# Kernel tuning notes

Hardware: AMD Instinct MI355X
Metric: run time of the kernel (lower is better)

Reference implementation:

```python
import jax, jax.numpy as jnp
import numpy as np

B, N, DIM, QK, H, GS = 4, 4096, 512, 512, 8, 128
NUM_LABELS = 8
R_BASE, R_MIN, R_MAX = 0.5, 0.25, 0.75
LAMBDA_P, LAMBDA_V, CCR = 0.25, 0.25, 0.125


def setup_inputs() -> dict:
    key = jax.random.key(0)
    ks = jax.random.split(key, 7)
    s = DIM ** -0.5
    return {
        "x": jax.random.normal(ks[0], (B, N, DIM), jnp.float32),
        "labels": jax.random.randint(ks[1], (B, N), 0, NUM_LABELS),
        "scores": jax.random.uniform(ks[2], (B, N), jnp.float32),
        "Wq": jax.random.normal(ks[3], (DIM, QK), jnp.float32) * s,
        "Wk": jax.random.normal(ks[4], (DIM, QK), jnp.float32) * s,
        "Wv": jax.random.normal(ks[5], (DIM, DIM), jnp.float32) * s,
        "Wproj": jax.random.normal(ks[6], (DIM, DIM), jnp.float32) * s,
    }


def _windows(t, gs, ng):
    # pad with flipped last-group tail, then overlapping windows of size 2*gs, stride gs
    tp = jnp.concatenate([t, jnp.flip(t[:, -gs:], axis=1)], axis=1)
    a = tp.reshape(t.shape[0], ng + 1, gs, *t.shape[2:])
    return jnp.concatenate([a[:, :-1], a[:, 1:]], axis=2)  # [b, ng, 2*gs, ...]


def _topk_mask(vals, keep, cand):
    # rank of each entry when sorted descending; keep top-`keep` among candidates
    ranks = jnp.argsort(jnp.argsort(-vals, axis=-1), axis=-1)
    return (ranks < keep[:, :, None, None, None]) & cand


def reference(x, labels, scores, Wq, Wk, Wv, Wproj):
    b, n, _ = x.shape
    gs = GS
    ng = n // gs            # num_tokens divisible by group_size -> pad_n = 0
    ws = 2 * gs
    q = x @ Wq
    k = x @ Wk
    v = x @ Wv

    qw = q.reshape(b, ng, gs, H, -1).transpose(0, 1, 3, 2, 4)          # b ng h gs d
    kw = _windows(k, gs, ng).reshape(b, ng, ws, H, -1).transpose(0, 1, 3, 2, 4)
    vw = _windows(v, gs, ng).reshape(b, ng, ws, H, -1).transpose(0, 1, 3, 2, 4)
    q_labels = labels.reshape(b, ng, gs)
    k_labels = _windows(labels, gs, ng)                                 # b ng ws
    q_scores = scores.reshape(b, ng, gs)
    k_scores = _windows(scores, gs, ng)

    d = qw.shape[-1]
    scale = 1.0 / jnp.sqrt(jnp.asarray(d, qw.dtype))
    logits = jnp.einsum('bghqd,bghkd->bghqk', qw, kw) * scale           # b ng h gs ws
    attn_hat = jax.nn.softmax(logits, axis=-1)  # no prev_attn_state -> attn_hat = attn_cur

    # dynamic focus ratio: purity from group mode label + score variance
    counts = jax.nn.one_hot(q_labels, NUM_LABELS, dtype=jnp.float32).sum(axis=2)  # b ng L
    mode = jnp.argmax(counts, axis=-1)
    purity = jnp.mean((q_labels == mode[..., None]).astype(jnp.float32), axis=-1)
    score_var = jnp.var(q_scores.astype(jnp.float32), axis=-1)  # unbiased=False
    focus = jnp.clip(R_BASE + LAMBDA_P * purity - LAMBDA_V * score_var, R_MIN, R_MAX)

    keep = jnp.clip(jnp.ceil(focus * ws).astype(jnp.int32), 1, ws)
    cross_keep = jnp.round(keep.astype(jnp.float32) * CCR).astype(jnp.int32)
    cross_keep = jnp.where(keep > 1, jnp.maximum(cross_keep, 1), 0)
    same_keep = jnp.maximum(keep - cross_keep, 1)

    same_mask = (q_labels[:, :, None, :, None] == k_labels[:, :, None, None, :])  # b ng 1 gs ws

    same_scores = jnp.where(same_mask, attn_hat, -10000.0)
    m_same = _topk_mask(same_scores, same_keep, same_mask)
    pair_conf = q_scores[:, :, None, :, None] * k_scores[:, :, None, None, :]
    cross_scores = attn_hat * pair_conf
    m_cross = _topk_mask(cross_scores, cross_keep, ~same_mask)
    final_mask = m_same | m_cross

    sparse_logits = jnp.where(final_mask, logits, -10000.0)
    attn_local = jax.nn.softmax(sparse_logits, axis=-1)
    attn_local = jnp.where(final_mask, attn_local, 0.0)
    attn_local = attn_local / (attn_local.sum(axis=-1, keepdims=True) + 1e-9)

    out = jnp.einsum('bghqk,bghkd->bghqd', attn_local, vw)
    out = out.transpose(0, 1, 3, 2, 4).reshape(b, ng * gs, -1)[:, :n]
    return out @ Wproj, attn_local
```

## Files before the change

### kernel.cpp

```cpp
#include <hip/hip_runtime.h>

#define BB 4
#define NN 4096
#define DIMM 512
#define HH 8
#define DH 64
#define GSZ 128
#define NGRP 32
#define WSZ 256
#define CHUNK 32

#define MK 8388608u
#define WK 262144u

typedef short short8 __attribute__((ext_vector_type(8)));
typedef float f32x4 __attribute__((ext_vector_type(4)));

__device__ inline unsigned short bf16rne(float f) {
  unsigned u = __float_as_uint(f);
  unsigned r = u + 0x7FFFu + ((u >> 16) & 1u);
  return (unsigned short)(r >> 16);
}
__device__ inline float bf16tof(unsigned short h) {
  return __uint_as_float(((unsigned)h) << 16);
}

__global__ __launch_bounds__(256) void split_planes(
    const float* __restrict__ X, unsigned short* __restrict__ P)
{
  unsigned idx = (blockIdx.x * 256u + threadIdx.x) * 4u;
  float4 xv = *(const float4*)&X[idx];
  float xs[4] = {xv.x, xv.y, xv.z, xv.w};
  ushort4 hv, mv, lv;
  unsigned short* hp = (unsigned short*)&hv;
  unsigned short* mp = (unsigned short*)&mv;
  unsigned short* lp = (unsigned short*)&lv;
#pragma unroll
  for (int i = 0; i < 4; ++i) {
    unsigned short h = bf16rne(xs[i]);
    float r1 = xs[i] - bf16tof(h);
    unsigned short m = bf16rne(r1);
    float r2 = r1 - bf16tof(m);
    hp[i] = h;
    mp[i] = m;
    lp[i] = bf16rne(r2);
  }
  *(ushort4*)&P[idx] = hv;
  *(ushort4*)&P[MK + idx] = mv;
  *(ushort4*)&P[2u * MK + idx] = lv;
}

__global__ __launch_bounds__(256) void split_w(
    const float* __restrict__ Wq, const float* __restrict__ Wk,
    const float* __restrict__ Wv, const float* __restrict__ Wpj,
    unsigned short* __restrict__ wqkv, unsigned short* __restrict__ wproj)
{
  unsigned e = blockIdx.x * 256u + threadIdx.x;
  int mz = e >> 18;
  unsigned rem = e & (WK - 1u);
  unsigned kk = rem >> 9, n = rem & 511u;
  const float* src = (mz == 0) ? Wq : (mz == 1) ? Wk : (mz == 2) ? Wv : Wpj;
  float w = src[kk * 512u + n];
  unsigned short h = bf16rne(w);
  float r1 = w - bf16tof(h);
  unsigned short m = bf16rne(r1);
  float r2 = r1 - bf16tof(m);
  unsigned short l = bf16rne(r2);
  unsigned o = n * 512u + kk;
  if (mz < 3) {
    unsigned short* base = wqkv + (unsigned)mz * 3u * WK;
    base[o] = h;
    base[WK + o] = m;
    base[2u * WK + o] = l;
  } else {
    wproj[o] = h;
    wproj[WK + o] = m;
  }
}

template <int NP, int NT>
__global__ __launch_bounds__(256) void mfma_gemm(
    const unsigned short* __restrict__ Ap,
    const unsigned short* __restrict__ Wp,
    float* __restrict__ C)
{
  constexpr int ta[6] = {0, 0, 1, 1, 0, 2};
  constexpr int tw[6] = {0, 1, 0, 1, 2, 0};
  const int z = blockIdx.z;
  const int n0 = blockIdx.x * 128;
  const int m0 = blockIdx.y * 128;
  const int tid = threadIdx.x;
  const int lane = tid & 63, wv = tid >> 6;
  const int wm = (wv >> 1) * 64, wn = (wv & 1) * 64;
  const int lm = lane & 15, lk = (lane >> 4) * 8;

  __shared__ unsigned short As[NP * 128 * 40];
  __shared__ unsigned short Ws[NP * 128 * 40];

  f32x4 acc[4][4];
#pragma unroll
  for (int i = 0; i < 4; ++i)
#pragma unroll
    for (int j = 0; j < 4; ++j) acc[i][j] = (f32x4){0.f, 0.f, 0.f, 0.f};

  const unsigned short* Wz = Wp + (size_t)z * NP * WK;

  for (int k0 = 0; k0 < 512; k0 += 32) {
#pragma unroll
    for (int i = 0; i < NP * 2; ++i) {
      int idx = i * 256 + tid;
      int p = idx >> 9, rem = idx & 511;
      int r = rem >> 2, cc = rem & 3;
      *(short8*)&As[p * 5120 + r * 40 + cc * 8] =
          *(const short8*)&Ap[(size_t)p * MK + (size_t)(m0 + r) * 512 + k0 + cc * 8];
      *(short8*)&Ws[p * 5120 + r * 40 + cc * 8] =
          *(const short8*)&Wz[(size_t)p * WK + (size_t)(n0 + r) * 512 + k0 + cc * 8];
    }
    __syncthreads();

    short8 a[NP][4];
#pragma unroll
    for (int p = 0; p < NP; ++p)
#pragma unroll
      for (int fm = 0; fm < 4; ++fm)
        a[p][fm] = *(const short8*)&As[p * 5120 + (wm + fm * 16 + lm) * 40 + lk];

#pragma unroll
    for (int fn = 0; fn < 4; ++fn) {
      short8 bf[NP];
#pragma unroll
      for (int p = 0; p < NP; ++p)
        bf[p] = *(const short8*)&Ws[p * 5120 + (wn + fn * 16 + lm) * 40 + lk];
#pragma unroll
      for (int fm = 0; fm < 4; ++fm) {
#pragma unroll
        for (int t = 0; t < NT; ++t)
          acc[fm][fn] = __builtin_amdgcn_mfma_f32_16x16x32_bf16(
              a[ta[t]][fm], bf[tw[t]], acc[fm][fn], 0, 0, 0);
      }
    }
    __syncthreads();
  }

  const int rq = (lane >> 4) * 4;
  float* Cz = C + (size_t)z * 8388608u;
#pragma unroll
  for (int fm = 0; fm < 4; ++fm)
#pragma unroll
    for (int fn = 0; fn < 4; ++fn) {
      int row = m0 + wm + fm * 16 + rq;
      int col = n0 + wn + fn * 16 + lm;
#pragma unroll
      for (int r = 0; r < 4; ++r)
        Cz[(size_t)(row + r) * 512 + col] = acc[fm][fn][r];
    }
}

__global__ __launch_bounds__(256) void gemm512(
    const float* __restrict__ A,
    const float* __restrict__ W0, const float* __restrict__ W1, const float* __restrict__ W2,
    float* __restrict__ C0, float* __restrict__ C1, float* __restrict__ C2)
{
  const int z = blockIdx.z;
  const float* Wm = (z == 0) ? W0 : (z == 1 ? W1 : W2);
  float* Cm = (z == 0) ? C0 : (z == 1 ? C1 : C2);
  const int n0 = blockIdx.x * 128;
  const int m0 = blockIdx.y * 128;
  const int tid = threadIdx.x;
  const int tx = tid & 15, ty = tid >> 4;

  __shared__ float As[32][132];
  __shared__ float Bs[32][132];

  float acc[8][8];
#pragma unroll
  for (int i = 0; i < 8; ++i)
#pragma unroll
    for (int j = 0; j < 8; ++j) acc[i][j] = 0.f;

  for (int k0 = 0; k0 < 512; k0 += 32) {
    {
      const int c4 = tid & 7, r = tid >> 3;
#pragma unroll
      for (int p = 0; p < 128; p += 32) {
        float4 av = *(const float4*)&A[(size_t)(m0 + r + p) * 512 + k0 + c4 * 4];
        As[c4 * 4 + 0][r + p] = av.x;
        As[c4 * 4 + 1][r + p] = av.y;
        As[c4 * 4 + 2][r + p] = av.z;
        As[c4 * 4 + 3][r + p] = av.w;
      }
      const int j4 = tid & 31, rb = tid >> 5;
#pragma unroll
      for (int p = 0; p < 32; p += 8) {
        *(float4*)&Bs[rb + p][j4 * 4] =
            *(const float4*)&Wm[(size_t)(k0 + rb + p) * 512 + n0 + j4 * 4];
      }
    }
    __syncthreads();
#pragma unroll
    for (int kk = 0; kk < 32; ++kk) {
      float4 a0 = *(const float4*)&As[kk][ty * 8];
      float4 a1 = *(const float4*)&As[kk][ty * 8 + 4];
      float4 b0 = *(const float4*)&Bs[kk][tx * 8];
      float4 b1 = *(const float4*)&Bs[kk][tx * 8 + 4];
      float av[8] = {a0.x, a0.y, a0.z, a0.w, a1.x, a1.y, a1.z, a1.w};
      float bv[8] = {b0.x, b0.y, b0.z, b0.w, b1.x, b1.y, b1.z, b1.w};
#pragma unroll
      for (int i = 0; i < 8; ++i)
#pragma unroll
        for (int j = 0; j < 8; ++j) acc[i][j] += av[i] * bv[j];
    }
    __syncthreads();
  }
#pragma unroll
  for (int i = 0; i < 8; ++i) {
    size_t row = (size_t)(m0 + ty * 8 + i);
    float4 o0 = make_float4(acc[i][0], acc[i][1], acc[i][2], acc[i][3]);
    float4 o1 = make_float4(acc[i][4], acc[i][5], acc[i][6], acc[i][7]);
    *(float4*)&Cm[row * 512 + n0 + tx * 8] = o0;
    *(float4*)&Cm[row * 512 + n0 + tx * 8 + 4] = o1;
  }
}

__device__ __forceinline__ void focus_keep(
    const int* klab, const float* kscr, int* hist8, float* s_var,
    int* s_sk, int* s_ck, int tid, int lane, int wv)
{
  if (tid < GSZ) atomicAdd(&hist8[klab[tid]], 1);
  if (wv == 0) {
    double x0 = (double)kscr[lane], x1 = (double)kscr[lane + 64];
    double s = x0 + x1;
#pragma unroll
    for (int off = 32; off > 0; off >>= 1) s += __shfl_xor(s, off);
    double mean = s * (1.0 / 128.0);
    double d0 = x0 - mean, d1 = x1 - mean;
    double vs = d0 * d0 + d1 * d1;
#pragma unroll
    for (int off = 32; off > 0; off >>= 1) vs += __shfl_xor(vs, off);
    if (lane == 0) *s_var = (float)(vs * (1.0 / 128.0));
  }
  __syncthreads();
  if (tid == 0) {
    int bc = hist8[0];
    for (int l = 1; l < 8; ++l)
      if (hist8[l] > bc) bc = hist8[l];
    float purity = (float)bc * (1.0f / GSZ);
    float focus = 0.5f + 0.25f * purity - 0.25f * (*s_var);
    focus = fminf(fmaxf(focus, 0.25f), 0.75f);
    int keep = (int)ceilf(focus * (float)WSZ);
    keep = min(max(keep, 1), WSZ);
    int ck = keep >> 3, rem = keep & 7;
    if (rem > 4 || (rem == 4 && (ck & 1))) ck++;
    if (ck < 1) ck = 1;
    int sk = keep - ck;
    if (sk < 1) sk = 1;
    *s_sk = sk;
    *s_ck = ck;
  }
  __syncthreads();
}

__device__ __forceinline__ void rank_rows(
    float att[CHUNK][WSZ + 4], const int* klab, const float* kscr,
    int r0, int same_keep, int cross_keep, int lane, int wv)
{
  int kl0[4];
  float ks0[4];
#pragma unroll
  for (int m = 0; m < 4; ++m) {
    kl0[m] = klab[lane + 64 * m];
    ks0[m] = kscr[lane + 64 * m];
  }
  for (int sp = 0; sp < 4; ++sp) {
    const int rA = wv * 8 + 2 * sp, rB = rA + 1;
    const int qLA = klab[r0 + rA], qLB = klab[r0 + rB];
    const float qSA = kscr[r0 + rA], qSB = kscr[r0 + rB];
    float aA[4], aB[4];
    float mxA = -INFINITY, mxB = -INFINITY;
#pragma unroll
    for (int m = 0; m < 4; ++m) {
      aA[m] = att[rA][lane + 64 * m];
      aB[m] = att[rB][lane + 64 * m];
      mxA = fmaxf(mxA, aA[m]);
      mxB = fmaxf(mxB, aB[m]);
    }
#pragma unroll
    for (int off = 32; off > 0; off >>= 1) {
      mxA = fmaxf(mxA, __shfl_xor(mxA, off));
      mxB = fmaxf(mxB, __shfl_xor(mxB, off));
    }
    unsigned fsA[4], fcA[4], fsB[4], fcB[4];
    bool cdA[4], cdB[4];
#pragma unroll
    for (int m = 0; m < 4; ++m) {
      aA[m] = expf(aA[m] - mxA);
      aB[m] = expf(aB[m] - mxB);
      cdA[m] = (kl0[m] == qLA);
      cdB[m] = (kl0[m] == qLB);
      fsA[m] = cdA[m] ? __float_as_uint(aA[m]) : 0u;
      fsB[m] = cdB[m] ? __float_as_uint(aB[m]) : 0u;
      fcA[m] = __float_as_uint(aA[m] * (qSA * ks0[m]));
      fcB[m] = __float_as_uint(aB[m] * (qSB * ks0[m]));
    }
    unsigned tsA = 0, tcA = 0, tsB = 0, tcB = 0;
    for (int bit = 29; bit >= 0; --bit) {
      unsigned csA = tsA | (1u << bit), ccA = tcA | (1u << bit);
      unsigned csB = tsB | (1u << bit), ccB = tcB | (1u << bit);
      int nsA = 0, ncA = 0, nsB = 0, ncB = 0;
#pragma unroll
      for (int m = 0; m < 4; ++m) {
        nsA += __popcll(__ballot(fsA[m] >= csA));
        ncA += __popcll(__ballot(fcA[m] >= ccA));
        nsB += __popcll(__ballot(fsB[m] >= csB));
        ncB += __popcll(__ballot(fcB[m] >= ccB));
      }
      if (nsA >= same_keep) tsA = csA;
      if (ncA >= cross_keep) tcA = ccA;
      if (nsB >= same_keep) tsB = csB;
      if (ncB >= cross_keep) tcB = ccB;
    }
#pragma unroll
    for (int rsel = 0; rsel < 2; ++rsel) {
      const int rr = rsel ? rB : rA;
      const unsigned ts = rsel ? tsB : tsA, tc = rsel ? tcB : tcA;
      unsigned* fs = rsel ? fsB : fsA;
      unsigned* fc = rsel ? fcB : fcA;
      float* a = rsel ? aB : aA;
      bool* cand = rsel ? cdB : cdA;
      unsigned long long beqs[4], beqc[4];
      int gts = 0, gtc = 0;
#pragma unroll
      for (int m = 0; m < 4; ++m) {
        gts += __popcll(__ballot(fs[m] > ts));
        gtc += __popcll(__ballot(fc[m] > tc));
        beqs[m] = __ballot(fs[m] == ts);
        beqc[m] = __ballot(fc[m] == tc);
      }
      const int rs = same_keep - gts, rc = cross_keep - gtc;
      float pv[4];
      float S = 0.f;
      int pres = 0, prec = 0;
#pragma unroll
      for (int m = 0; m < 4; ++m) {
        int mbs = __builtin_amdgcn_mbcnt_hi((unsigned)(beqs[m] >> 32),
                   __builtin_amdgcn_mbcnt_lo((unsigned)beqs[m], 0));
        int mbc = __builtin_amdgcn_mbcnt_hi((unsigned)(beqc[m] >> 32),
                   __builtin_amdgcn_mbcnt_lo((unsigned)beqc[m], 0));
        bool keep_s = cand[m] && ((fs[m] > ts) || ((fs[m] == ts) && (pres + mbs < rs)));
        bool keep_c = (!cand[m]) && ((fc[m] > tc) || ((fc[m] == tc) && (prec + mbc < rc)));
        pv[m] = (keep_s || keep_c) ? a[m] : 0.f;
        S += pv[m];
        pres += __popcll(beqs[m]);
        prec += __popcll(beqc[m]);
      }
#pragma unroll
      for (int off = 32; off > 0; off >>= 1) S += __shfl_xor(S, off);
      const float inv = 1.0f / S;
#pragma unroll
      for (int m = 0; m < 4; ++m) att[rr][lane + 64 * m] = pv[m] * inv;
    }
  }
}

template <int OMODE>
__global__ __launch_bounds__(256, 3) void attn_f32(
    const float* q, const float* __restrict__ k, const float* __restrict__ v,
    const int* __restrict__ labels, const float* __restrict__ scores,
    float* __restrict__ attn_out, float* o, unsigned short* __restrict__ opl)
{
  const int bx = blockIdx.x;
  const int c = bx >> 10;
  const int rblk = bx & 1023;
  const int h = rblk & 7;
  const int g = (rblk >> 3) & 31;
  const int b = rblk >> 8;
  const int r0 = c * CHUNK;
  const int tid = threadIdx.x;
  const int lane = tid & 63, wv = tid >> 6;

  __shared__ float att[CHUNK][WSZ + 4];
  __shared__ float ktile[64][DH + 4];
  __shared__ int klab[WSZ];
  __shared__ float kscr[WSZ];
  __shared__ int hist8[8];
  __shared__ float s_var;
  __shared__ int s_sk, s_ck;

  {
    int j = tid;
    int pos = g * GSZ + j;
    int tok = pos < NN ? pos : (2 * NN - 1 - pos);
    klab[j] = labels[b * NN + tok];
    kscr[j] = scores[b * NN + tok];
  }
  if (tid < 8) hist8[tid] = 0;
  __syncthreads();
  focus_keep(klab, kscr, hist8, &s_var, &s_sk, &s_ck, tid, lane, wv);
  const int same_keep = s_sk, cross_keep = s_ck;

  const int rp = tid >> 4, jx = tid & 15;
  const int srow = tid >> 4, sd4 = (tid & 15) * 4;
  const float* q0p = q + (size_t)(b * NN + g * GSZ + r0 + rp) * DIMM + h * DH;
  const float* q1p = q0p + (size_t)16 * DIMM;

  for (int jt = 0; jt < 4; ++jt) {
#pragma unroll
    for (int p = 0; p < 64; p += 16) {
      int j = jt * 64 + srow + p;
      int pos = g * GSZ + j;
      int tok = pos < NN ? pos : (2 * NN - 1 - pos);
      *(float4*)&ktile[srow + p][sd4] =
          *(const float4*)&k[(size_t)(b * NN + tok) * DIMM + h * DH + sd4];
    }
    __syncthreads();
    float acc0[4] = {0.f, 0.f, 0.f, 0.f}, acc1[4] = {0.f, 0.f, 0.f, 0.f};
#pragma unroll
    for (int dd = 0; dd < DH; dd += 4) {
      float4 q0 = *(const float4*)(q0p + dd);
      float4 q1 = *(const float4*)(q1p + dd);
#pragma unroll
      for (int jj = 0; jj < 4; ++jj) {
        float4 kv = *(const float4*)&ktile[jx + 16 * jj][dd];
        acc0[jj] += q0.x * kv.x + q0.y * kv.y + q0.z * kv.z + q0.w * kv.w;
        acc1[jj] += q1.x * kv.x + q1.y * kv.y + q1.z * kv.z + q1.w * kv.w;
      }
    }
#pragma unroll
    for (int jj = 0; jj < 4; ++jj) {
      att[rp][jt * 64 + jx + 16 * jj] = acc0[jj] * 0.125f;
      att[rp + 16][jt * 64 + jx + 16 * jj] = acc1[jj] * 0.125f;
    }
    __syncthreads();
  }

  rank_rows(att, klab, kscr, r0, same_keep, cross_keep, lane, wv);
  __syncthreads();

  {
    size_t base = ((((size_t)b * NGRP + g) * HH + h) * GSZ + r0) * WSZ;
#pragma unroll
    for (int it = 0; it < 8; ++it) {
      int idx = it * 256 + tid;
      int i = idx >> 6, j4 = (idx & 63) * 4;
      *(float4*)&attn_out[base + (size_t)i * WSZ + j4] = *(float4*)&att[i][j4];
    }
  }

  const int dx = jx;
  float oa0[4] = {0.f, 0.f, 0.f, 0.f}, oa1[4] = {0.f, 0.f, 0.f, 0.f};
  for (int jt = 0; jt < 4; ++jt) {
#pragma unroll
    for (int p = 0; p < 64; p += 16) {
      int j = jt * 64 + srow + p;
      int pos = g * GSZ + j;
      int tok = pos < NN ? pos : (2 * NN - 1 - pos);
      *(float4*)&ktile[srow + p][sd4] =
          *(const float4*)&v[(size_t)(b * NN + tok) * DIMM + h * DH + sd4];
    }
    __syncthreads();
#pragma unroll 4
    for (int jg = 0; jg < 16; ++jg) {
      float4 p0 = *(const float4*)&att[rp][jt * 64 + jg * 4];
      float4 p1 = *(const float4*)&att[rp + 16][jt * 64 + jg * 4];
      float4 v0 = *(const float4*)&ktile[jg * 4 + 0][dx * 4];
      float4 v1 = *(const float4*)&ktile[jg * 4 + 1][dx * 4];
      float4 v2 = *(const float4*)&ktile[jg * 4 + 2][dx * 4];
      float4 v3 = *(const float4*)&ktile[jg * 4 + 3][dx * 4];
      oa0[0] += p0.x * v0.x + p0.y * v1.x + p0.z * v2.x + p0.w * v3.x;
      oa0[1] += p0.x * v0.y + p0.y * v1.y + p0.z * v2.y + p0.w * v3.y;
      oa0[2] += p0.x * v0.z + p0.y * v1.z + p0.z * v2.z + p0.w * v3.z;
      oa0[3] += p0.x * v0.w + p0.y * v1.w + p0.z * v2.w + p0.w * v3.w;
      oa1[0] += p1.x * v0.x + p1.y * v1.x + p1.z * v2.x + p1.w * v3.x;
      oa1[1] += p1.x * v0.y + p1.y * v1.y + p1.z * v2.y + p1.w * v3.y;
      oa1[2] += p1.x * v0.z + p1.y * v1.z + p1.z * v2.z + p1.w * v3.z;
      oa1[3] += p1.x * v0.w + p1.y * v1.w + p1.z * v2.w + p1.w * v3.w;
    }
    __syncthreads();
  }
  if (OMODE == 0) {
    size_t ob0 = (size_t)(b * NN + g * GSZ + r0 + rp) * DIMM + h * DH + dx * 4;
    *(float4*)&o[ob0] = make_float4(oa0[0], oa0[1], oa0[2], oa0[3]);
    *(float4*)&o[ob0 + (size_t)16 * DIMM] = make_float4(oa1[0], oa1[1], oa1[2], oa1[3]);
  } else {
    size_t ob0 = (size_t)(b * NN + g * GSZ + r0 + rp) * 512 + h * 64 + dx * 4;
    ushort4 h0, m0v, h1, m1v;
    unsigned short* h0p = (unsigned short*)&h0;
    unsigned short* m0p = (unsigned short*)&m0v;
    unsigned short* h1p = (unsigned short*)&h1;
    unsigned short* m1p = (unsigned short*)&m1v;
#pragma unroll
    for (int i = 0; i < 4; ++i) {
      unsigned short hh = bf16rne(oa0[i]);
      h0p[i] = hh;
      m0p[i] = bf16rne(oa0[i] - bf16tof(hh));
      unsigned short hh1 = bf16rne(oa1[i]);
      h1p[i] = hh1;
      m1p[i] = bf16rne(oa1[i] - bf16tof(hh1));
    }
    *(ushort4*)&opl[ob0] = h0;
    *(ushort4*)&opl[MK + ob0] = m0v;
    *(ushort4*)&opl[ob0 + 16 * 512] = h1;
    *(ushort4*)&opl[MK + ob0 + 16 * 512] = m1v;
  }
}

extern "C" void kernel_launch(void* const* d_in, const int* in_sizes, int n_in,
                              void* d_out, int out_size, void* d_ws, size_t ws_size,
                              hipStream_t stream) {
  const float* x      = (const float*)d_in[0];
  const int*   labels = (const int*)d_in[1];
  const float* scores = (const float*)d_in[2];
  const float* Wq     = (const float*)d_in[3];
  const float* Wk     = (const float*)d_in[4];
  const float* Wv     = (const float*)d_in[5];
  const float* Wproj  = (const float*)d_in[6];

  float* out = (float*)d_out;
  float* attn_out = out + (size_t)BB * NN * DIMM;

  float* qb = (float*)d_ws;
  float* kb = qb + (size_t)MK;
  float* vf = kb + (size_t)MK;
  unsigned short* xpl  = (unsigned short*)(vf + (size_t)MK);
  unsigned short* wqkv = xpl + 3 * (size_t)MK;
  unsigned short* wpp  = wqkv + 9 * (size_t)WK;
  const size_t required = 3 * (size_t)MK * 4 + 3 * (size_t)MK * 2 + 11 * (size_t)WK * 2;

  if (ws_size >= required) {
    split_planes<<<dim3(MK / 1024), 256, 0, stream>>>(x, xpl);
    split_w<<<dim3(4 * WK / 256), 256, 0, stream>>>(Wq, Wk, Wv, Wproj, wqkv, wpp);
    mfma_gemm<3, 6><<<dim3(4, 128, 2), 256, 0, stream>>>(xpl, wqkv, qb);
    mfma_gemm<2, 3><<<dim3(4, 128, 1), 256, 0, stream>>>(xpl, wqkv + 6 * (size_t)WK, vf);
    attn_f32<1><<<dim3(BB * NGRP * HH * 4), 256, 0, stream>>>(
        qb, kb, vf, labels, scores, attn_out, nullptr, xpl);
    mfma_gemm<2, 3><<<dim3(4, 128, 1), 256, 0, stream>>>(xpl, wpp, out);
  } else {
    const size_t SZ = (size_t)BB * NN * DIMM;
    float* q2 = (float*)d_ws;
    float* k2 = q2 + SZ;
    float* v2 = k2 + SZ;
    gemm512<<<dim3(4, 128, 3), 256, 0, stream>>>(x, Wq, Wk, Wv, q2, k2, v2);
    attn_f32<0><<<dim3(BB * NGRP * HH * 4), 256, 0, stream>>>(
        q2, k2, v2, labels, scores, attn_out, q2, nullptr);
    gemm512<<<dim3(4, 128, 1), 256, 0, stream>>>(q2, Wproj, Wproj, Wproj, out, out, out);
  }
}
```

Baseline: 811.0 us.

## Use split-bf16 MFMA for attention-times-V and write probabilities directly

Adds a new attention kernel whose P·V product runs on bf16 MFMA with hi/lo split planes (three products) instead of scalar fp32 FMAs. V tiles are loaded, split into bf16 hi/lo and stored transposed in shared memory that aliases the K tile buffer. Probabilities are written straight from registers to global memory, and labels are stored as bytes in shared memory. This trades exact fp32 accumulation for a three-term bf16 approximation and adds conversion work and extra shared-memory traffic.

```diff
diff --git a/kernel.cpp b/kernel.cpp
--- a/kernel.cpp
+++ b/kernel.cpp
@@ -223,7 +223,7 @@
 }
 
 __device__ __forceinline__ void focus_keep(
-    const int* klab, const float* kscr, int* hist8, float* s_var,
+    const unsigned char* klab, const float* kscr, int* hist8, float* s_var,
     int* s_sk, int* s_ck, int tid, int lane, int wv)
 {
   if (tid < GSZ) atomicAdd(&hist8[klab[tid]], 1);
@@ -260,113 +260,11 @@
   __syncthreads();
 }
 
-__device__ __forceinline__ void rank_rows(
-    float att[CHUNK][WSZ + 4], const int* klab, const float* kscr,
-    int r0, int same_keep, int cross_keep, int lane, int wv)
-{
-  int kl0[4];
-  float ks0[4];
-#pragma unroll
-  for (int m = 0; m < 4; ++m) {
-    kl0[m] = klab[lane + 64 * m];
-    ks0[m] = kscr[lane + 64 * m];
-  }
-  for (int sp = 0; sp < 4; ++sp) {
-    const int rA = wv * 8 + 2 * sp, rB = rA + 1;
-    const int qLA = klab[r0 + rA], qLB = klab[r0 + rB];
-    const float qSA = kscr[r0 + rA], qSB = kscr[r0 + rB];
-    float aA[4], aB[4];
-    float mxA = -INFINITY, mxB = -INFINITY;
-#pragma unroll
-    for (int m = 0; m < 4; ++m) {
-      aA[m] = att[rA][lane + 64 * m];
-      aB[m] = att[rB][lane + 64 * m];
-      mxA = fmaxf(mxA, aA[m]);
-      mxB = fmaxf(mxB, aB[m]);
-    }
-#pragma unroll
-    for (int off = 32; off > 0; off >>= 1) {
-      mxA = fmaxf(mxA, __shfl_xor(mxA, off));
-      mxB = fmaxf(mxB, __shfl_xor(mxB, off));
-    }
-    unsigned fsA[4], fcA[4], fsB[4], fcB[4];
-    bool cdA[4], cdB[4];
-#pragma unroll
-    for (int m = 0; m < 4; ++m) {
-      aA[m] = expf(aA[m] - mxA);
-      aB[m] = expf(aB[m] - mxB);
-      cdA[m] = (kl0[m] == qLA);
-      cdB[m] = (kl0[m] == qLB);
-      fsA[m] = cdA[m] ? __float_as_uint(aA[m]) : 0u;
-      fsB[m] = cdB[m] ? __float_as_uint(aB[m]) : 0u;
-      fcA[m] = __float_as_uint(aA[m] * (qSA * ks0[m]));
-      fcB[m] = __float_as_uint(aB[m] * (qSB * ks0[m]));
-    }
-    unsigned tsA = 0, tcA = 0, tsB = 0, tcB = 0;
-    for (int bit = 29; bit >= 0; --bit) {
-      unsigned csA = tsA | (1u << bit), ccA = tcA | (1u << bit);
-      unsigned csB = tsB | (1u << bit), ccB = tcB | (1u << bit);
-      int nsA = 0, ncA = 0, nsB = 0, ncB = 0;
-#pragma unroll
-      for (int m = 0; m < 4; ++m) {
-        nsA += __popcll(__ballot(fsA[m] >= csA));
-        ncA += __popcll(__ballot(fcA[m] >= ccA));
-        nsB += __popcll(__ballot(fsB[m] >= csB));
-        ncB += __popcll(__ballot(fcB[m] >= ccB));
-      }
-      if (nsA >= same_keep) tsA = csA;
-      if (ncA >= cross_keep) tcA = ccA;
-      if (nsB >= same_keep) tsB = csB;
-      if (ncB >= cross_keep) tcB = ccB;
-    }
-#pragma unroll
-    for (int rsel = 0; rsel < 2; ++rsel) {
-      const int rr = rsel ? rB : rA;
-      const unsigned ts = rsel ? tsB : tsA, tc = rsel ? tcB : tcA;
-      unsigned* fs = rsel ? fsB : fsA;
-      unsigned* fc = rsel ? fcB : fcA;
-      float* a = rsel ? aB : aA;
-      bool* cand = rsel ? cdB : cdA;
-      unsigned long long beqs[4], beqc[4];
-      int gts = 0, gtc = 0;
-#pragma unroll
-      for (int m = 0; m < 4; ++m) {
-        gts += __popcll(__ballot(fs[m] > ts));
-        gtc += __popcll(__ballot(fc[m] > tc));
-        beqs[m] = __ballot(fs[m] == ts);
-        beqc[m] = __ballot(fc[m] == tc);
-      }
-      const int rs = same_keep - gts, rc = cross_keep - gtc;
-      float pv[4];
-      float S = 0.f;
-      int pres = 0, prec = 0;
-#pragma unroll
-      for (int m = 0; m < 4; ++m) {
-        int mbs = __builtin_amdgcn_mbcnt_hi((unsigned)(beqs[m] >> 32),
-                   __builtin_amdgcn_mbcnt_lo((unsigned)beqs[m], 0));
-        int mbc = __builtin_amdgcn_mbcnt_hi((unsigned)(beqc[m] >> 32),
-                   __builtin_amdgcn_mbcnt_lo((unsigned)beqc[m], 0));
-        bool keep_s = cand[m] && ((fs[m] > ts) || ((fs[m] == ts) && (pres + mbs < rs)));
-        bool keep_c = (!cand[m]) && ((fc[m] > tc) || ((fc[m] == tc) && (prec + mbc < rc)));
-        pv[m] = (keep_s || keep_c) ? a[m] : 0.f;
-        S += pv[m];
-        pres += __popcll(beqs[m]);
-        prec += __popcll(beqc[m]);
-      }
-#pragma unroll
-      for (int off = 32; off > 0; off >>= 1) S += __shfl_xor(S, off);
-      const float inv = 1.0f / S;
-#pragma unroll
-      for (int m = 0; m < 4; ++m) att[rr][lane + 64 * m] = pv[m] * inv;
-    }
-  }
-}
-
-template <int OMODE>
-__global__ __launch_bounds__(256, 3) void attn_f32(
-    const float* q, const float* __restrict__ k, const float* __restrict__ v,
+__global__ __launch_bounds__(256, 3) void attn_v9(
+    const float* __restrict__ q, const float* __restrict__ k,
+    const float* __restrict__ vf,
     const int* __restrict__ labels, const float* __restrict__ scores,
-    float* __restrict__ attn_out, float* o, unsigned short* __restrict__ opl)
+    float* __restrict__ attn_out, unsigned short* __restrict__ opl)
 {
   const int bx = blockIdx.x;
   const int c = bx >> 10;
@@ -377,10 +275,13 @@
   const int r0 = c * CHUNK;
   const int tid = threadIdx.x;
   const int lane = tid & 63, wv = tid >> 6;
-
-  __shared__ float att[CHUNK][WSZ + 4];
-  __shared__ float ktile[64][DH + 4];
-  __shared__ int klab[WSZ];
+  const int lm = lane & 15, lq = lane >> 4;
+
+  __shared__ float att[CHUNK][264];
+  __shared__ __align__(16) unsigned char vbuf[18432];
+  float (*ktile)[68] = (float (*)[68])vbuf;
+  unsigned short* vtT = (unsigned short*)vbuf;
+  __shared__ unsigned char klab[WSZ];
   __shared__ float kscr[WSZ];
   __shared__ int hist8[8];
   __shared__ float s_var;
@@ -390,7 +291,7 @@
     int j = tid;
     int pos = g * GSZ + j;
     int tok = pos < NN ? pos : (2 * NN - 1 - pos);
-    klab[j] = labels[b * NN + tok];
+    klab[j] = (unsigned char)labels[b * NN + tok];
     kscr[j] = scores[b * NN + tok];
   }
   if (tid < 8) hist8[tid] = 0;
@@ -433,18 +334,356 @@
     __syncthreads();
   }
 
-  rank_rows(att, klab, kscr, r0, same_keep, cross_keep, lane, wv);
+  {
+    int kl0[4];
+    float ks0[4];
+#pragma unroll
+    for (int m = 0; m < 4; ++m) {
+      kl0[m] = klab[lane + 64 * m];
+      ks0[m] = kscr[lane + 64 * m];
+    }
+    for (int sp = 0; sp < 4; ++sp) {
+      const int rA = wv * 8 + 2 * sp, rB = rA + 1;
+      const int qLA = klab[r0 + rA], qLB = klab[r0 + rB];
+      const float qSA = kscr[r0 + rA], qSB = kscr[r0 + rB];
+      float aA[4], aB[4];
+      float mxA = -INFINITY, mxB = -INFINITY;
+#pragma unroll
+      for (int m = 0; m < 4; ++m) {
+        aA[m] = att[rA][lane + 64 * m];
+        aB[m] = att[rB][lane + 64 * m];
+        mxA = fmaxf(mxA, aA[m]);
+        mxB = fmaxf(mxB, aB[m]);
+      }
+#pragma unroll
+      for (int off = 32; off > 0; off >>= 1) {
+        mxA = fmaxf(mxA, __shfl_xor(mxA, off));
+        mxB = fmaxf(mxB, __shfl_xor(mxB, off));
+      }
+      unsigned fsA[4], fcA[4], fsB[4], fcB[4];
+      bool cdA[4], cdB[4];
+#pragma unroll
+      for (int m = 0; m < 4; ++m) {
+        aA[m] = expf(aA[m] - mxA);
+        aB[m] = expf(aB[m] - mxB);
+        cdA[m] = (kl0[m] == qLA);
+        cdB[m] = (kl0[m] == qLB);
+        fsA[m] = cdA[m] ? __float_as_uint(aA[m]) : 0u;
+        fsB[m] = cdB[m] ? __float_as_uint(aB[m]) : 0u;
+        fcA[m] = __float_as_uint(aA[m] * (qSA * ks0[m]));
+        fcB[m] = __float_as_uint(aB[m] * (qSB * ks0[m]));
+      }
+      unsigned tsA = 0, tcA = 0, tsB = 0, tcB = 0;
+      for (int bit = 29; bit >= 0; --bit) {
+        unsigned csA = tsA | (1u << bit), ccA = tcA | (1u << bit);
+        unsigned csB = tsB | (1u << bit), ccB = tcB | (1u << bit);
+        int nsA = 0, ncA = 0, nsB = 0, ncB = 0;
+#pragma unroll
+        for (int m = 0; m < 4; ++m) {
+          nsA += __popcll(__ballot(fsA[m] >= csA));
+          ncA += __popcll(__ballot(fcA[m] >= ccA));
+          nsB += __popcll(__ballot(fsB[m] >= csB));
+          ncB += __popcll(__ballot(fcB[m] >= ccB));
+        }
+        if (nsA >= same_keep) tsA = csA;
+        if (ncA >= cross_keep) tcA = ccA;
+        if (nsB >= same_keep) tsB = csB;
+        if (ncB >= cross_keep) tcB = ccB;
+      }
+#pragma unroll
+      for (int rsel = 0; rsel < 2; ++rsel) {
+        const int rr = rsel ? rB : rA;
+        const unsigned ts = rsel ? tsB : tsA, tc = rsel ? tcB : tcA;
+        unsigned* fs = rsel ? fsB : fsA;
+        unsigned* fc = rsel ? fcB : fcA;
+        float* a = rsel ? aB : aA;
+        bool* cand = rsel ? cdB : cdA;
+        unsigned long long beqs[4], beqc[4];
+        int gts = 0, gtc = 0;
+#pragma unroll
+        for (int m = 0; m < 4; ++m) {
+          gts += __popcll(__ballot(fs[m] > ts));
+          gtc += __popcll(__ballot(fc[m] > tc));
+          beqs[m] = __ballot(fs[m] == ts);
+          beqc[m] = __ballot(fc[m] == tc);
+        }
+        const int rs = same_keep - gts, rc = cross_keep - gtc;
+        float pv[4];
+        float S = 0.f;
+        int pres = 0, prec = 0;
+#pragma unroll
+        for (int m = 0; m < 4; ++m) {
+          int mbs = __builtin_amdgcn_mbcnt_hi((unsigned)(beqs[m] >> 32),
+                     __builtin_amdgcn_mbcnt_lo((unsigned)beqs[m], 0));
+          int mbc = __builtin_amdgcn_mbcnt_hi((unsigned)(beqc[m] >> 32),
+                     __builtin_amdgcn_mbcnt_lo((unsigned)beqc[m], 0));
+          bool keep_s = cand[m] && ((fs[m] > ts) || ((fs[m] == ts) && (pres + mbs < rs)));
+          bool keep_c = (!cand[m]) && ((fc[m] > tc) || ((fc[m] == tc) && (prec + mbc < rc)));
+          pv[m] = (keep_s || keep_c) ? a[m] : 0.f;
+          S += pv[m];
+          pres += __popcll(beqs[m]);
+          prec += __popcll(beqc[m]);
+        }
+#pragma unroll
+        for (int off = 32; off > 0; off >>= 1) S += __shfl_xor(S, off);
+        const float inv = 1.0f / S;
+        size_t gb = ((((size_t)b * NGRP + g) * HH + h) * GSZ + (r0 + rr)) * WSZ + lane;
+        unsigned short* prow = (unsigned short*)&att[rr][0];
+#pragma unroll
+        for (int m = 0; m < 4; ++m) {
+          float p = pv[m] * inv;
+          attn_out[gb + 64 * m] = p;
+          unsigned short hh = bf16rne(p);
+          prow[lane + 64 * m] = hh;
+          prow[264 + lane + 64 * m] = bf16rne(p - bf16tof(hh));
+        }
+      }
+    }
+  }
+
+  f32x4 acc2[2] = {(f32x4){0.f, 0.f, 0.f, 0.f}, (f32x4){0.f, 0.f, 0.f, 0.f}};
+  for (int jt = 0; jt < 4; ++jt) {
+    __syncthreads();
+    {
+      const int dx_ = tid & 15, jh = tid >> 4;
+#pragma unroll
+      for (int ps = 0; ps < 2; ++ps) {
+        int jl0 = ps * 32 + 2 * jh;
+        float4 v0, v1;
+#pragma unroll
+        for (int qq = 0; qq < 2; ++qq) {
+          int pos = g * GSZ + jt * 64 + jl0 + qq;
+          int tok = pos < NN ? pos : (2 * NN - 1 - pos);
+          float4 vv = *(const float4*)&vf[(size_t)(b * NN + tok) * DIMM + h * DH + dx_ * 4];
+          if (qq == 0) v0 = vv; else v1 = vv;
+        }
+        const float* a0 = (const float*)&v0;
+        const float* a1 = (const float*)&v1;
+#pragma unroll
+        for (int i = 0; i < 4; ++i) {
+          int d = dx_ * 4 + i;
+          unsigned short h0 = bf16rne(a0[i]);
+          unsigned short h1 = bf16rne(a1[i]);
+          unsigned short m0 = bf16rne(a0[i] - bf16tof(h0));
+          unsigned short m1 = bf16rne(a1[i] - bf16tof(h1));
+          *(unsigned*)&vtT[0 * 4608 + d * 72 + jl0] = (unsigned)h0 | ((unsigned)h1 << 16);
+          *(unsigned*)&vtT[1 * 4608 + d * 72 + jl0] = (unsigned)m0 | ((unsigned)m1 << 16);
+        }
+      }
+    }
+    __syncthreads();
+#pragma unroll
+    for (int kt = 0; kt < 2; ++kt) {
+      const int koff = jt * 64 + kt * 32 + lq * 8;
+      short8 ahi[2], ami[2];
+#pragma unroll
+      for (int mt = 0; mt < 2; ++mt) {
+        const unsigned short* arow = (const unsigned short*)&att[mt * 16 + lm][0];
+        ahi[mt] = *(const short8*)&arow[koff];
+        ami[mt] = *(const short8*)&arow[264 + koff];
+      }
+      const int vo = (wv * 16 + lm) * 72 + kt * 32 + lq * 8;
+      short8 bhi = *(const short8*)&vtT[vo];
+      short8 bmi = *(const short8*)&vtT[4608 + vo];
+#pragma unroll
+      for (int mt = 0; mt < 2; ++mt) {
+        acc2[mt] = __builtin_amdgcn_mfma_f32_16x16x32_bf16(ahi[mt], bhi, acc2[mt], 0, 0, 0);
+        acc2[mt] = __builtin_amdgcn_mfma_f32_16x16x32_bf16(ahi[mt], bmi, acc2[mt], 0, 0, 0);
+        acc2[mt] = __builtin_amdgcn_mfma_f32_16x16x32_bf16(ami[mt], bhi, acc2[mt], 0, 0, 0);
+      }
+    }
+  }
+
+  {
+    size_t rowbase = (size_t)(b * NN + g * GSZ + r0);
+#pragma unroll
+    for (int mt = 0; mt < 2; ++mt)
+#pragma unroll
+      for (int r = 0; r < 4; ++r) {
+        int row = mt * 16 + lq * 4 + r;
+        float val = acc2[mt][r];
+        unsigned short hh = bf16rne(val);
+        size_t oaddr = (rowbase + row) * 512 + h * 64 + wv * 16 + lm;
+        opl[oaddr] = hh;
+        opl[MK + oaddr] = bf16rne(val - bf16tof(hh));
+      }
+  }
+}
+
+__global__ __launch_bounds__(256, 3) void attn_f32(
+    const float* q, const float* __restrict__ k, const float* __restrict__ v,
+    const int* __restrict__ labels, const float* __restrict__ scores,
+    float* __restrict__ attn_out, float* o)
+{
+  const int bx = blockIdx.x;
+  const int c = bx >> 10;
+  const int rblk = bx & 1023;
+  const int h = rblk & 7;
+  const int g = (rblk >> 3) & 31;
+  const int b = rblk >> 8;
+  const int r0 = c * CHUNK;
+  const int tid = threadIdx.x;
+  const int lane = tid & 63, wv = tid >> 6;
+
+  __shared__ float att[CHUNK][WSZ + 4];
+  __shared__ float ktile[64][DH + 4];
+  __shared__ unsigned char klab[WSZ];
+  __shared__ float kscr[WSZ];
+  __shared__ int hist8[8];
+  __shared__ float s_var;
+  __shared__ int s_sk, s_ck;
+
+  {
+    int j = tid;
+    int pos = g * GSZ + j;
+    int tok = pos < NN ? pos : (2 * NN - 1 - pos);
+    klab[j] = (unsigned char)labels[b * NN + tok];
+    kscr[j] = scores[b * NN + tok];
+  }
+  if (tid < 8) hist8[tid] = 0;
   __syncthreads();
+  focus_keep(klab, kscr, hist8, &s_var, &s_sk, &s_ck, tid, lane, wv);
+  const int same_keep = s_sk, cross_keep = s_ck;
+
+  const int rp = tid >> 4, jx = tid & 15;
+  const int srow = tid >> 4, sd4 = (tid & 15) * 4;
+  const float* q0p = q + (size_t)(b * NN + g * GSZ + r0 + rp) * DIMM + h * DH;
+  const float* q1p = q0p + (size_t)16 * DIMM;
+
+  for (int jt = 0; jt < 4; ++jt) {
+#pragma unroll
+    for (int p = 0; p < 64; p += 16) {
+      int j = jt * 64 + srow + p;
+      int pos = g * GSZ + j;
+      int tok = pos < NN ? pos : (2 * NN - 1 - pos);
+      *(float4*)&ktile[srow + p][sd4] =
+          *(const float4*)&k[(size_t)(b * NN + tok) * DIMM + h * DH + sd4];
+    }
+    __syncthreads();
+    float acc0[4] = {0.f, 0.f, 0.f, 0.f}, acc1[4] = {0.f, 0.f, 0.f, 0.f};
+#pragma unroll
+    for (int dd = 0; dd < DH; dd += 4) {
+      float4 q0 = *(const float4*)(q0p + dd);
+      float4 q1 = *(const float4*)(q1p + dd);
+#pragma unroll
+      for (int jj = 0; jj < 4; ++jj) {
+        float4 kv = *(const float4*)&ktile[jx + 16 * jj][dd];
+        acc0[jj] += q0.x * kv.x + q0.y * kv.y + q0.z * kv.z + q0.w * kv.w;
+        acc1[jj] += q1.x * kv.x + q1.y * kv.y + q1.z * kv.z + q1.w * kv.w;
+      }
+    }
+#pragma unroll
+    for (int jj = 0; jj < 4; ++jj) {
+      att[rp][jt * 64 + jx + 16 * jj] = acc0[jj] * 0.125f;
+      att[rp + 16][jt * 64 + jx + 16 * jj] = acc1[jj] * 0.125f;
+    }
+    __syncthreads();
+  }
 
   {
-    size_t base = ((((size_t)b * NGRP + g) * HH + h) * GSZ + r0) * WSZ;
-#pragma unroll
-    for (int it = 0; it < 8; ++it) {
-      int idx = it * 256 + tid;
-      int i = idx >> 6, j4 = (idx & 63) * 4;
-      *(float4*)&attn_out[base + (size_t)i * WSZ + j4] = *(float4*)&att[i][j4];
-    }
-  }
+    int kl0[4];
+    float ks0[4];
+#pragma unroll
+    for (int m = 0; m < 4; ++m) {
+      kl0[m] = klab[lane + 64 * m];
+      ks0[m] = kscr[lane + 64 * m];
+    }
+    for (int sp = 0; sp < 4; ++sp) {
+      const int rA = wv * 8 + 2 * sp, rB = rA + 1;
+      const int qLA = klab[r0 + rA], qLB = klab[r0 + rB];
+      const float qSA = kscr[r0 + rA], qSB = kscr[r0 + rB];
+      float aA[4], aB[4];
+      float mxA = -INFINITY, mxB = -INFINITY;
+#pragma unroll
+      for (int m = 0; m < 4; ++m) {
+        aA[m] = att[rA][lane + 64 * m];
+        aB[m] = att[rB][lane + 64 * m];
+        mxA = fmaxf(mxA, aA[m]);
+        mxB = fmaxf(mxB, aB[m]);
+      }
+#pragma unroll
+      for (int off = 32; off > 0; off >>= 1) {
+        mxA = fmaxf(mxA, __shfl_xor(mxA, off));
+        mxB = fmaxf(mxB, __shfl_xor(mxB, off));
+      }
+      unsigned fsA[4], fcA[4], fsB[4], fcB[4];
+      bool cdA[4], cdB[4];
+#pragma unroll
+      for (int m = 0; m < 4; ++m) {
+        aA[m] = expf(aA[m] - mxA);
+        aB[m] = expf(aB[m] - mxB);
+        cdA[m] = (kl0[m] == qLA);
+        cdB[m] = (kl0[m] == qLB);
+        fsA[m] = cdA[m] ? __float_as_uint(aA[m]) : 0u;
+        fsB[m] = cdB[m] ? __float_as_uint(aB[m]) : 0u;
+        fcA[m] = __float_as_uint(aA[m] * (qSA * ks0[m]));
+        fcB[m] = __float_as_uint(aB[m] * (qSB * ks0[m]));
+      }
+      unsigned tsA = 0, tcA = 0, tsB = 0, tcB = 0;
+      for (int bit = 29; bit >= 0; --bit) {
+        unsigned csA = tsA | (1u << bit), ccA = tcA | (1u << bit);
+        unsigned csB = tsB | (1u << bit), ccB = tcB | (1u << bit);
+        int nsA = 0, ncA = 0, nsB = 0, ncB = 0;
+#pragma unroll
+        for (int m = 0; m < 4; ++m) {
+          nsA += __popcll(__ballot(fsA[m] >= csA));
+          ncA += __popcll(__ballot(fcA[m] >= ccA));
+          nsB += __popcll(__ballot(fsB[m] >= csB));
+          ncB += __popcll(__ballot(fcB[m] >= ccB));
+        }
+        if (nsA >= same_keep) tsA = csA;
+        if (ncA >= cross_keep) tcA = ccA;
+        if (nsB >= same_keep) tsB = csB;
+        if (ncB >= cross_keep) tcB = ccB;
+      }
+#pragma unroll
+      for (int rsel = 0; rsel < 2; ++rsel) {
+        const int rr = rsel ? rB : rA;
+        const unsigned ts = rsel ? tsB : tsA, tc = rsel ? tcB : tcA;
+        unsigned* fs = rsel ? fsB : fsA;
+        unsigned* fc = rsel ? fcB : fcA;
+        float* a = rsel ? aB : aA;
+        bool* cand = rsel ? cdB : cdA;
+        unsigned long long beqs[4], beqc[4];
+        int gts = 0, gtc = 0;
+#pragma unroll
+        for (int m = 0; m < 4; ++m) {
+          gts += __popcll(__ballot(fs[m] > ts));
+          gtc += __popcll(__ballot(fc[m] > tc));
+          beqs[m] = __ballot(fs[m] == ts);
+          beqc[m] = __ballot(fc[m] == tc);
+        }
+        const int rs = same_keep - gts, rc = cross_keep - gtc;
+        float pv[4];
+        float S = 0.f;
+        int pres = 0, prec = 0;
+#pragma unroll
+        for (int m = 0; m < 4; ++m) {
+          int mbs = __builtin_amdgcn_mbcnt_hi((unsigned)(beqs[m] >> 32),
+                     __builtin_amdgcn_mbcnt_lo((unsigned)beqs[m], 0));
+          int mbc = __builtin_amdgcn_mbcnt_hi((unsigned)(beqc[m] >> 32),
+                     __builtin_amdgcn_mbcnt_lo((unsigned)beqc[m], 0));
+          bool keep_s = cand[m] && ((fs[m] > ts) || ((fs[m] == ts) && (pres + mbs < rs)));
+          bool keep_c = (!cand[m]) && ((fc[m] > tc) || ((fc[m] == tc) && (prec + mbc < rc)));
+          pv[m] = (keep_s || keep_c) ? a[m] : 0.f;
+          S += pv[m];
+          pres += __popcll(beqs[m]);
+          prec += __popcll(beqc[m]);
+        }
+#pragma unroll
+        for (int off = 32; off > 0; off >>= 1) S += __shfl_xor(S, off);
+        const float inv = 1.0f / S;
+        size_t gb = ((((size_t)b * NGRP + g) * HH + h) * GSZ + (r0 + rr)) * WSZ + lane;
+#pragma unroll
+        for (int m = 0; m < 4; ++m) {
+          float p = pv[m] * inv;
+          att[rr][lane + 64 * m] = p;
+          attn_out[gb + 64 * m] = p;
+        }
+      }
+    }
+  }
+  __syncthreads();
 
   const int dx = jx;
   float oa0[4] = {0.f, 0.f, 0.f, 0.f}, oa1[4] = {0.f, 0.f, 0.f, 0.f};
@@ -477,30 +716,10 @@
     }
     __syncthreads();
   }
-  if (OMODE == 0) {
+  {
     size_t ob0 = (size_t)(b * NN + g * GSZ + r0 + rp) * DIMM + h * DH + dx * 4;
     *(float4*)&o[ob0] = make_float4(oa0[0], oa0[1], oa0[2], oa0[3]);
     *(float4*)&o[ob0 + (size_t)16 * DIMM] = make_float4(oa1[0], oa1[1], oa1[2], oa1[3]);
-  } else {
-    size_t ob0 = (size_t)(b * NN + g * GSZ + r0 + rp) * 512 + h * 64 + dx * 4;
-    ushort4 h0, m0v, h1, m1v;
-    unsigned short* h0p = (unsigned short*)&h0;
-    unsigned short* m0p = (unsigned short*)&m0v;
-    unsigned short* h1p = (unsigned short*)&h1;
-    unsigned short* m1p = (unsigned short*)&m1v;
-#pragma unroll
-    for (int i = 0; i < 4; ++i) {
-      unsigned short hh = bf16rne(oa0[i]);
-      h0p[i] = hh;
-      m0p[i] = bf16rne(oa0[i] - bf16tof(hh));
-      unsigned short hh1 = bf16rne(oa1[i]);
-      h1p[i] = hh1;
-      m1p[i] = bf16rne(oa1[i] - bf16tof(hh1));
-    }
-    *(ushort4*)&opl[ob0] = h0;
-    *(ushort4*)&opl[MK + ob0] = m0v;
-    *(ushort4*)&opl[ob0 + 16 * 512] = h1;
-    *(ushort4*)&opl[MK + ob0 + 16 * 512] = m1v;
   }
 }
 
@@ -531,8 +750,8 @@
     split_w<<<dim3(4 * WK / 256), 256, 0, stream>>>(Wq, Wk, Wv, Wproj, wqkv, wpp);
     mfma_gemm<3, 6><<<dim3(4, 128, 2), 256, 0, stream>>>(xpl, wqkv, qb);
     mfma_gemm<2, 3><<<dim3(4, 128, 1), 256, 0, stream>>>(xpl, wqkv + 6 * (size_t)WK, vf);
-    attn_f32<1><<<dim3(BB * NGRP * HH * 4), 256, 0, stream>>>(
-        qb, kb, vf, labels, scores, attn_out, nullptr, xpl);
+    attn_v9<<<dim3(BB * NGRP * HH * 4), 256, 0, stream>>>(
+        qb, kb, vf, labels, scores, attn_out, xpl);
     mfma_gemm<2, 3><<<dim3(4, 128, 1), 256, 0, stream>>>(xpl, wpp, out);
   } else {
     const size_t SZ = (size_t)BB * NN * DIMM;
@@ -540,8 +759,8 @@
     float* k2 = q2 + SZ;
     float* v2 = k2 + SZ;
     gemm512<<<dim3(4, 128, 3), 256, 0, stream>>>(x, Wq, Wk, Wv, q2, k2, v2);
-    attn_f32<0><<<dim3(BB * NGRP * HH * 4), 256, 0, stream>>>(
-        q2, k2, v2, labels, scores, attn_out, q2, nullptr);
+    attn_f32<<<dim3(BB * NGRP * HH * 4), 256, 0, stream>>>(
+        q2, k2, v2, labels, scores, attn_out, q2);
     gemm512<<<dim3(4, 128, 1), 256, 0, stream>>>(q2, Wproj, Wproj, Wproj, out, out, out);
   }
 }
```

Result: faster. 745.2 us (-8.1%).
